# Performance work log

Hardware: AMD Instinct MI355X
Metric: run time of the kernel (lower is better)

Reference implementation:

```python
import jax, jax.numpy as jnp
import numpy as np

NUM_HEADS = 12


def setup_inputs() -> dict:
    key = jax.random.key(0)
    k1, k2, k3 = jax.random.split(key, 3)
    B, N, C = 4, 2048, 768
    x = jax.random.normal(k1, (B, N, C), dtype=jnp.float32)
    # Linear weights stored as [in, out] so y = x @ W (+ b); matches torch Linear math.
    w_qkv = jax.random.normal(k2, (C, 3 * C), dtype=jnp.float32) * (C ** -0.5)
    w_proj = jax.random.normal(k3, (C, C), dtype=jnp.float32) * (C ** -0.5)
    b_proj = jnp.zeros((C,), dtype=jnp.float32)
    return {"x": x, "w_qkv": w_qkv, "w_proj": w_proj, "b_proj": b_proj}


def reference(x, w_qkv, w_proj, b_proj):
    B, N, C = x.shape
    H = NUM_HEADS
    D = C // H
    scale = D ** -0.5
    qkv = (x @ w_qkv).reshape(B, N, 3, H, D)
    qkv = jnp.transpose(qkv, (2, 0, 3, 1, 4))  # [3, B, H, N, D]
    q, k, v = qkv[0], qkv[1], qkv[2]
    attn = jnp.einsum("bhnd,bhmd->bhnm", q, k) * scale  # [B, H, N, N]
    # causal mask (triu with offset 1), filled with -finfo.max as in the torch code
    causal_mask = jnp.triu(jnp.ones((N, N), dtype=bool), k=1)
    mask_value = -jnp.finfo(attn.dtype).max
    attn = jnp.where(causal_mask, mask_value, attn)
    attn = jax.nn.softmax(attn, axis=-1)
    attn = jnp.nan_to_num(attn)
    out = jnp.einsum("bhnm,bhmd->bhnd", attn, v)  # [B, H, N, D]
    out = jnp.transpose(out, (0, 2, 1, 3)).reshape(B, N, C)
    return out @ w_proj + b_proj
```

## Files before the change

kernel.cpp:

```cpp
#include <hip/hip_runtime.h>
#include <hip/hip_bf16.h>
#include <math.h>

#define BATCH 4
#define SEQ   2048
#define CDIM  768
#define NHEAD 12
#define HDIM  64
#define MROWS (BATCH*SEQ)
#define QKVC  (3*CDIM)

typedef __bf16    bf16x8 __attribute__((ext_vector_type(8)));
typedef _Float16  f16x8  __attribute__((ext_vector_type(8)));
typedef _Float16  f16x4  __attribute__((ext_vector_type(4)));
typedef float     f32x4  __attribute__((ext_vector_type(4)));

__device__ __forceinline__ void async16(const void* g, void* l) {
  __builtin_amdgcn_global_load_lds(
      (const __attribute__((address_space(1))) void*)g,
      (__attribute__((address_space(3))) void*)l, 16, 0, 0);
}

__global__ __launch_bounds__(256) void cast_f32_bf16(
    const float* __restrict__ in, __bf16* __restrict__ out, int n8) {
  int i = blockIdx.x * 256 + threadIdx.x;
  if (i >= n8) return;
  float4 a = reinterpret_cast<const float4*>(in)[i * 2];
  float4 b = reinterpret_cast<const float4*>(in)[i * 2 + 1];
  bf16x8 o;
  o[0] = (__bf16)a.x; o[1] = (__bf16)a.y; o[2] = (__bf16)a.z; o[3] = (__bf16)a.w;
  o[4] = (__bf16)b.x; o[5] = (__bf16)b.y; o[6] = (__bf16)b.z; o[7] = (__bf16)b.w;
  reinterpret_cast<bf16x8*>(out)[i] = o;
}

__global__ __launch_bounds__(256) void transpose_cast(
    const float* __restrict__ w, __bf16* __restrict__ wt, int K, int N) {
  __shared__ float sh[32][33];
  const int n0 = blockIdx.x * 32, k0 = blockIdx.y * 32;
  const int tx = threadIdx.x, ty = threadIdx.y;
#pragma unroll
  for (int i = 0; i < 4; ++i)
    sh[ty + i * 8][tx] = w[(size_t)(k0 + ty + i * 8) * N + n0 + tx];
  __syncthreads();
#pragma unroll
  for (int i = 0; i < 4; ++i)
    wt[(size_t)(n0 + ty + i * 8) * K + k0 + tx] = (__bf16)sh[tx][ty + i * 8];
}

template <int MODE>
__global__ __launch_bounds__(256) void gemm_bk64_kernel(
    const __bf16* __restrict__ A, const __bf16* __restrict__ Bt,
    const float* __restrict__ bias, void* __restrict__ Cout,
    __bf16* __restrict__ kF, _Float16* __restrict__ vF,
    int M, int N, int K) {
  __shared__ __align__(16) __bf16 As[2][128 * 32];
  __shared__ __align__(16) __bf16 Bs[2][128 * 32];
  const int tid  = threadIdx.x;
  const int w    = tid >> 6;
  const int lane = tid & 63;
  const int quad = lane >> 4;
  const int lr   = lane & 15;
  const int wr   = w >> 1, wc = w & 1;
  const int mBase = blockIdx.y * 128, nBase = blockIdx.x * 128;

  f32x4 acc[4][4] = {};

  const int srow = lane >> 2;
  const int sk8  = (lane & 3) * 8;
  const __bf16* aSrc0 = A  + (size_t)(mBase + w * 32 + srow) * K + sk8;
  const __bf16* aSrc1 = aSrc0 + (size_t)16 * K;
  const __bf16* bSrc0 = Bt + (size_t)(nBase + w * 32 + srow) * K + sk8;
  const __bf16* bSrc1 = bSrc0 + (size_t)16 * K;

  for (int k0 = 0; k0 < K; k0 += 64) {
    __syncthreads();
#pragma unroll
    for (int kh = 0; kh < 2; ++kh) {
      async16(aSrc0 + k0 + kh * 32, &As[kh][(w * 32 + 0) * 32]);
      async16(aSrc1 + k0 + kh * 32, &As[kh][(w * 32 + 16) * 32]);
      async16(bSrc0 + k0 + kh * 32, &Bs[kh][(w * 32 + 0) * 32]);
      async16(bSrc1 + k0 + kh * 32, &Bs[kh][(w * 32 + 16) * 32]);
    }
    __syncthreads();

#pragma unroll
    for (int kh = 0; kh < 2; ++kh) {
      bf16x8 af[4], bfr[4];
#pragma unroll
      for (int mt = 0; mt < 4; ++mt)
        af[mt] = *reinterpret_cast<const bf16x8*>(
            &As[kh][(wr * 64 + mt * 16 + lr) * 32 + quad * 8]);
#pragma unroll
      for (int nt = 0; nt < 4; ++nt)
        bfr[nt] = *reinterpret_cast<const bf16x8*>(
            &Bs[kh][(wc * 64 + nt * 16 + lr) * 32 + quad * 8]);
#pragma unroll
      for (int mt = 0; mt < 4; ++mt)
#pragma unroll
        for (int nt = 0; nt < 4; ++nt)
          acc[mt][nt] = __builtin_amdgcn_mfma_f32_16x16x32_bf16(
              af[mt], bfr[nt], acc[mt][nt], 0, 0, 0);
    }
  }

  if (MODE == 1) {
#pragma unroll
    for (int mt = 0; mt < 4; ++mt)
#pragma unroll
      for (int nt = 0; nt < 4; ++nt) {
        const int col = nBase + wc * 64 + nt * 16 + lr;
#pragma unroll
        for (int r = 0; r < 4; ++r) {
          const size_t row = (size_t)(mBase + wr * 64 + mt * 16 + quad * 4 + r);
          ((float*)Cout)[row * N + col] = acc[mt][nt][r] + bias[col];
        }
      }
  } else {
    const int region = nBase / CDIM;
    if (region == 0) {
#pragma unroll
      for (int mt = 0; mt < 4; ++mt)
#pragma unroll
        for (int nt = 0; nt < 4; ++nt) {
          const int col = nBase + wc * 64 + nt * 16 + lr;
#pragma unroll
          for (int r = 0; r < 4; ++r) {
            const size_t row = (size_t)(mBase + wr * 64 + mt * 16 + quad * 4 + r);
            ((__bf16*)Cout)[row * N + col] = (__bf16)acc[mt][nt][r];
          }
        }
    } else {
      const int bb  = mBase >> 11;
      const int ktB = ((mBase & 2047) >> 6) + wr;
      const int hq  = ((nBase % CDIM) + wc * 64) >> 6;
      const size_t tile = ((size_t)(bb * NHEAD + hq) * 32 + ktB) * 4096;
      if (region == 1) {
#pragma unroll
        for (int mt = 0; mt < 4; ++mt)
#pragma unroll
          for (int nt = 0; nt < 4; ++nt) {
            const size_t base = tile + (size_t)(mt * 2 + (nt >> 1)) * 512
                + (((nt & 1) * 2 + (lr >> 3)) * 16) * 8 + (lr & 7);
#pragma unroll
            for (int r = 0; r < 4; ++r)
              kF[base + (quad * 4 + r) * 8] = (__bf16)acc[mt][nt][r];
          }
      } else {
#pragma unroll
        for (int mt = 0; mt < 4; ++mt)
#pragma unroll
          for (int nt = 0; nt < 4; ++nt) {
            f16x4 vp;
#pragma unroll
            for (int r = 0; r < 4; ++r) vp[r] = (_Float16)acc[mt][nt][r];
            *reinterpret_cast<f16x4*>(
                &vF[tile + (size_t)(mt * 2 + (nt >> 1)) * 512
                    + (quad * 16 + lr) * 8 + (nt & 1) * 4]) = vp;
          }
      }
    }
  }
}

__global__ __launch_bounds__(256, 2) void flash_mfma_kernel(
    const __bf16* __restrict__ qkv, const __bf16* __restrict__ kF,
    const _Float16* __restrict__ vF, __bf16* __restrict__ out) {
  const int bid  = blockIdx.x;
  const int tid  = threadIdx.x;
  const int w    = tid >> 6;
  const int lane = tid & 63;
  const int quad = lane >> 4;
  const int lr   = lane & 15;

  const int x   = bid & 7;
  const int g   = bid >> 3;
  const int qt  = 31 - (g / 6);
  const int hb  = x * 6 + (g % 6);
  const int h   = hb % NHEAD, b = hb / NHEAD;

  __shared__ __align__(16) float Red[2][64 * 80];

  bf16x8 qf[4][2];
  {
    const float qs = 0.125f * 1.44269504088896f;
    const __bf16* qp = qkv + (size_t)(b * SEQ + qt * 64) * QKVC + h * HDIM;
#pragma unroll
    for (int qg = 0; qg < 4; ++qg)
#pragma unroll
      for (int kc = 0; kc < 2; ++kc) {
        bf16x8 qr = *reinterpret_cast<const bf16x8*>(
            qp + (size_t)(qg * 16 + lr) * QKVC + kc * 32 + quad * 8);
        bf16x8 f;
#pragma unroll
        for (int j = 0; j < 8; ++j) f[j] = (__bf16)((float)qr[j] * qs);
        qf[qg][kc] = f;
      }
  }

  f32x4 O[4][4] = {};
  f32x4 O4[4] = {};

  const __bf16*   kT = kF + ((size_t)(hb * 32)) * 4096 + lane * 8;
  const _Float16* vT = vF + ((size_t)(hb * 32)) * 4096 + lane * 8;
  const f16x4 vones = {(_Float16)1.f, (_Float16)1.f, (_Float16)1.f, (_Float16)1.f};

  for (int kt = w; kt <= qt; kt += 4) {
    bf16x8 kf[8];
    f16x8  vf8[8];
#pragma unroll
    for (int f = 0; f < 8; ++f)
      kf[f] = *reinterpret_cast<const bf16x8*>(kT + (size_t)kt * 4096 + f * 512);
#pragma unroll
    for (int gg = 0; gg < 8; ++gg)
      vf8[gg] = *reinterpret_cast<const f16x8*>(vT + (size_t)kt * 4096 + gg * 512);

#pragma unroll
    for (int nt = 0; nt < 4; ++nt) {
      f32x4 s[4];
#pragma unroll
      for (int qg = 0; qg < 4; ++qg) {
        f32x4 acc = (f32x4){0.f, 0.f, 0.f, 0.f};
        acc = __builtin_amdgcn_mfma_f32_16x16x32_bf16(kf[nt * 2 + 0], qf[qg][0], acc, 0, 0, 0);
        acc = __builtin_amdgcn_mfma_f32_16x16x32_bf16(kf[nt * 2 + 1], qf[qg][1], acc, 0, 0, 0);
        s[qg] = acc;
      }
      if (kt == qt) {
#pragma unroll
        for (int qg = 0; qg < 4; ++qg)
#pragma unroll
          for (int r = 0; r < 4; ++r)
            if (nt * 16 + quad * 4 + r > qg * 16 + lr) s[qg][r] = -1e30f;
      }
      f16x4 pa[4];
#pragma unroll
      for (int qg = 0; qg < 4; ++qg) {
        f16x4 t;
#pragma unroll
        for (int r = 0; r < 4; ++r)
          t[r] = (_Float16)__builtin_amdgcn_exp2f(s[qg][r]);
        pa[qg] = t;
      }
#pragma unroll
      for (int qg = 0; qg < 4; ++qg)
        O4[qg] = __builtin_amdgcn_mfma_f32_16x16x16f16(pa[qg], vones, O4[qg], 0, 0, 0);
#pragma unroll
      for (int dt = 0; dt < 4; ++dt) {
        const f16x8 vv = vf8[nt * 2 + (dt >> 1)];
        f16x4 vb;
#pragma unroll
        for (int j = 0; j < 4; ++j) vb[j] = vv[(dt & 1) * 4 + j];
#pragma unroll
        for (int qg = 0; qg < 4; ++qg)
          O[qg][dt] = __builtin_amdgcn_mfma_f32_16x16x16f16(pa[qg], vb, O[qg][dt], 0, 0, 0);
      }
    }
  }

  if (w == 1 || w == 3) {
    float* dst = Red[w >> 1];
#pragma unroll
    for (int qg = 0; qg < 4; ++qg)
#pragma unroll
      for (int dt = 0; dt < 4; ++dt)
        *reinterpret_cast<f32x4*>(&dst[((qg * 4 + dt) * 64 + lane) * 4]) = O[qg][dt];
#pragma unroll
    for (int qg = 0; qg < 4; ++qg)
      *reinterpret_cast<f32x4*>(&dst[((16 + qg) * 64 + lane) * 4]) = O4[qg];
  }
  __syncthreads();
  if (w == 0 || w == 2) {
    const float* src = Red[w >> 1];
#pragma unroll
    for (int qg = 0; qg < 4; ++qg)
#pragma unroll
      for (int dt = 0; dt < 4; ++dt)
        O[qg][dt] += *reinterpret_cast<const f32x4*>(&src[((qg * 4 + dt) * 64 + lane) * 4]);
#pragma unroll
    for (int qg = 0; qg < 4; ++qg)
      O4[qg] += *reinterpret_cast<const f32x4*>(&src[((16 + qg) * 64 + lane) * 4]);
  }
  __syncthreads();
  if (w == 2) {
    float* dst = Red[0];
#pragma unroll
    for (int qg = 0; qg < 4; ++qg)
#pragma unroll
      for (int dt = 0; dt < 4; ++dt)
        *reinterpret_cast<f32x4*>(&dst[((qg * 4 + dt) * 64 + lane) * 4]) = O[qg][dt];
#pragma unroll
    for (int qg = 0; qg < 4; ++qg)
      *reinterpret_cast<f32x4*>(&dst[((16 + qg) * 64 + lane) * 4]) = O4[qg];
  }
  __syncthreads();
  if (w == 0) {
    const float* src = Red[0];
#pragma unroll
    for (int qg = 0; qg < 4; ++qg)
#pragma unroll
      for (int dt = 0; dt < 4; ++dt)
        O[qg][dt] += *reinterpret_cast<const f32x4*>(&src[((qg * 4 + dt) * 64 + lane) * 4]);
#pragma unroll
    for (int qg = 0; qg < 4; ++qg)
      O4[qg] += *reinterpret_cast<const f32x4*>(&src[((16 + qg) * 64 + lane) * 4]);

    __bf16* obase = out + (size_t)(b * SEQ + qt * 64) * CDIM + h * HDIM;
#pragma unroll
    for (int qg = 0; qg < 4; ++qg) {
      float linv[4];
#pragma unroll
      for (int r = 0; r < 4; ++r) linv[r] = 1.f / O4[qg][r];
#pragma unroll
      for (int dt = 0; dt < 4; ++dt)
#pragma unroll
        for (int r = 0; r < 4; ++r)
          obase[(size_t)(qg * 16 + quad * 4 + r) * CDIM + dt * 16 + lr] =
              (__bf16)(O[qg][dt][r] * linv[r]);
    }
  }
}

extern "C" void kernel_launch(void* const* d_in, const int* in_sizes, int n_in,
                              void* d_out, int out_size, void* d_ws, size_t ws_size,
                              hipStream_t stream) {
  const float* x      = (const float*)d_in[0];
  const float* w_qkv  = (const float*)d_in[1];
  const float* w_proj = (const float*)d_in[2];
  const float* b_proj = (const float*)d_in[3];
  float* out = (float*)d_out;

  __bf16* qkv    = (__bf16*)d_ws;
  __bf16* attnb  = qkv + (size_t)MROWS * QKVC;
  __bf16* xb     = attnb + (size_t)MROWS * CDIM;
  __bf16* wqkvT  = xb + (size_t)MROWS * CDIM;
  __bf16* wprojT = wqkvT + (size_t)QKVC * CDIM;
  __bf16* kFb    = wprojT + (size_t)CDIM * CDIM;
  _Float16* vFb  = (_Float16*)(kFb + (size_t)48 * 32 * 4096);

  cast_f32_bf16<<<dim3((MROWS * CDIM / 8 + 255) / 256), dim3(256), 0, stream>>>(
      x, xb, MROWS * CDIM / 8);
  transpose_cast<<<dim3(QKVC / 32, CDIM / 32), dim3(32, 8), 0, stream>>>(
      w_qkv, wqkvT, CDIM, QKVC);
  transpose_cast<<<dim3(CDIM / 32, CDIM / 32), dim3(32, 8), 0, stream>>>(
      w_proj, wprojT, CDIM, CDIM);

  gemm_bk64_kernel<0><<<dim3(QKVC / 128, MROWS / 128), dim3(256), 0, stream>>>(
      xb, wqkvT, nullptr, qkv, kFb, vFb, MROWS, QKVC, CDIM);

  flash_mfma_kernel<<<dim3(1536), dim3(256), 0, stream>>>(qkv, kFb, vFb, attnb);

  gemm_bk64_kernel<1><<<dim3(CDIM / 128, MROWS / 128), dim3(256), 0, stream>>>(
      attnb, wprojT, b_proj, out, nullptr, nullptr, MROWS, CDIM, CDIM);
}
```

Baseline: 195.3 us.

## Pair causal query tiles per block, merge prep kernels, pack exp conversion

The flash attention kernel now processes two query tiles per block (tile 31-p and tile p), so every block does a balanced amount of causal work and the grid is halved to 768 blocks. The three preprocessing launches (x cast and two weight transposes) are merged into one prep kernel to cut launch overhead. The exp-to-half conversion uses packed round-toward-zero cvt_pkrtz instead of per-element casts. The trade-off is fewer blocks for the scheduler to spread across CUs, a slight rounding change in the probabilities, and an extra barrier per phase.

```diff
diff --git a/kernel.cpp b/kernel.cpp
--- a/kernel.cpp
+++ b/kernel.cpp
@@ -14,6 +14,7 @@
 typedef _Float16  f16x8  __attribute__((ext_vector_type(8)));
 typedef _Float16  f16x4  __attribute__((ext_vector_type(4)));
 typedef float     f32x4  __attribute__((ext_vector_type(4)));
+typedef __fp16    hf16x2 __attribute__((ext_vector_type(2)));
 
 __device__ __forceinline__ void async16(const void* g, void* l) {
   __builtin_amdgcn_global_load_lds(
@@ -21,30 +22,44 @@
       (__attribute__((address_space(3))) void*)l, 16, 0, 0);
 }
 
-__global__ __launch_bounds__(256) void cast_f32_bf16(
-    const float* __restrict__ in, __bf16* __restrict__ out, int n8) {
-  int i = blockIdx.x * 256 + threadIdx.x;
-  if (i >= n8) return;
-  float4 a = reinterpret_cast<const float4*>(in)[i * 2];
-  float4 b = reinterpret_cast<const float4*>(in)[i * 2 + 1];
-  bf16x8 o;
-  o[0] = (__bf16)a.x; o[1] = (__bf16)a.y; o[2] = (__bf16)a.z; o[3] = (__bf16)a.w;
-  o[4] = (__bf16)b.x; o[5] = (__bf16)b.y; o[6] = (__bf16)b.z; o[7] = (__bf16)b.w;
-  reinterpret_cast<bf16x8*>(out)[i] = o;
-}
-
-__global__ __launch_bounds__(256) void transpose_cast(
-    const float* __restrict__ w, __bf16* __restrict__ wt, int K, int N) {
+__global__ __launch_bounds__(256) void prep_kernel(
+    const float* __restrict__ x, __bf16* __restrict__ xb,
+    const float* __restrict__ w_qkv, __bf16* __restrict__ wqkvT,
+    const float* __restrict__ w_proj, __bf16* __restrict__ wprojT) {
   __shared__ float sh[32][33];
-  const int n0 = blockIdx.x * 32, k0 = blockIdx.y * 32;
-  const int tx = threadIdx.x, ty = threadIdx.y;
+  const int bid = blockIdx.x;
+  const int tid = threadIdx.x;
+
+  if (bid < 3072) {
+    const int i = bid * 256 + tid;
+    float4 a = reinterpret_cast<const float4*>(x)[i * 2];
+    float4 b = reinterpret_cast<const float4*>(x)[i * 2 + 1];
+    bf16x8 o;
+    o[0] = (__bf16)a.x; o[1] = (__bf16)a.y; o[2] = (__bf16)a.z; o[3] = (__bf16)a.w;
+    o[4] = (__bf16)b.x; o[5] = (__bf16)b.y; o[6] = (__bf16)b.z; o[7] = (__bf16)b.w;
+    reinterpret_cast<bf16x8*>(xb)[i] = o;
+    return;
+  }
+  const float* w;
+  __bf16* wt;
+  int n0, k0, N;
+  if (bid < 4800) {
+    const int t = bid - 3072;
+    w = w_qkv; wt = wqkvT; N = QKVC;
+    n0 = (t % 72) * 32; k0 = (t / 72) * 32;
+  } else {
+    const int t = bid - 4800;
+    w = w_proj; wt = wprojT; N = CDIM;
+    n0 = (t % 24) * 32; k0 = (t / 24) * 32;
+  }
+  const int tx = tid & 31, ty = tid >> 5;
 #pragma unroll
   for (int i = 0; i < 4; ++i)
     sh[ty + i * 8][tx] = w[(size_t)(k0 + ty + i * 8) * N + n0 + tx];
   __syncthreads();
 #pragma unroll
   for (int i = 0; i < 4; ++i)
-    wt[(size_t)(n0 + ty + i * 8) * K + k0 + tx] = (__bf16)sh[tx][ty + i * 8];
+    wt[(size_t)(n0 + ty + i * 8) * CDIM + k0 + tx] = (__bf16)sh[tx][ty + i * 8];
 }
 
 template <int MODE>
@@ -174,147 +189,153 @@
 
   const int x   = bid & 7;
   const int g   = bid >> 3;
-  const int qt  = 31 - (g / 6);
+  const int p   = g / 6;
   const int hb  = x * 6 + (g % 6);
   const int h   = hb % NHEAD, b = hb / NHEAD;
 
   __shared__ __align__(16) float Red[2][64 * 80];
-
-  bf16x8 qf[4][2];
-  {
-    const float qs = 0.125f * 1.44269504088896f;
-    const __bf16* qp = qkv + (size_t)(b * SEQ + qt * 64) * QKVC + h * HDIM;
-#pragma unroll
-    for (int qg = 0; qg < 4; ++qg)
-#pragma unroll
-      for (int kc = 0; kc < 2; ++kc) {
-        bf16x8 qr = *reinterpret_cast<const bf16x8*>(
-            qp + (size_t)(qg * 16 + lr) * QKVC + kc * 32 + quad * 8);
-        bf16x8 f;
-#pragma unroll
-        for (int j = 0; j < 8; ++j) f[j] = (__bf16)((float)qr[j] * qs);
-        qf[qg][kc] = f;
-      }
-  }
-
-  f32x4 O[4][4] = {};
-  f32x4 O4[4] = {};
 
   const __bf16*   kT = kF + ((size_t)(hb * 32)) * 4096 + lane * 8;
   const _Float16* vT = vF + ((size_t)(hb * 32)) * 4096 + lane * 8;
   const f16x4 vones = {(_Float16)1.f, (_Float16)1.f, (_Float16)1.f, (_Float16)1.f};
 
-  for (int kt = w; kt <= qt; kt += 4) {
-    bf16x8 kf[8];
-    f16x8  vf8[8];
-#pragma unroll
-    for (int f = 0; f < 8; ++f)
-      kf[f] = *reinterpret_cast<const bf16x8*>(kT + (size_t)kt * 4096 + f * 512);
-#pragma unroll
-    for (int gg = 0; gg < 8; ++gg)
-      vf8[gg] = *reinterpret_cast<const f16x8*>(vT + (size_t)kt * 4096 + gg * 512);
-
-#pragma unroll
-    for (int nt = 0; nt < 4; ++nt) {
-      f32x4 s[4];
+  for (int phase = 0; phase < 2; ++phase) {
+    const int qt = phase ? p : 31 - p;
+
+    bf16x8 qf[4][2];
+    {
+      const float qs = 0.125f * 1.44269504088896f;
+      const __bf16* qp = qkv + (size_t)(b * SEQ + qt * 64) * QKVC + h * HDIM;
+#pragma unroll
+      for (int qg = 0; qg < 4; ++qg)
+#pragma unroll
+        for (int kc = 0; kc < 2; ++kc) {
+          bf16x8 qr = *reinterpret_cast<const bf16x8*>(
+              qp + (size_t)(qg * 16 + lr) * QKVC + kc * 32 + quad * 8);
+          bf16x8 f;
+#pragma unroll
+          for (int j = 0; j < 8; ++j) f[j] = (__bf16)((float)qr[j] * qs);
+          qf[qg][kc] = f;
+        }
+    }
+
+    f32x4 O[4][4] = {};
+    f32x4 O4[4] = {};
+
+    for (int kt = w; kt <= qt; kt += 4) {
+      bf16x8 kf[8];
+      f16x8  vf8[8];
+#pragma unroll
+      for (int f = 0; f < 8; ++f)
+        kf[f] = *reinterpret_cast<const bf16x8*>(kT + (size_t)kt * 4096 + f * 512);
+#pragma unroll
+      for (int gg = 0; gg < 8; ++gg)
+        vf8[gg] = *reinterpret_cast<const f16x8*>(vT + (size_t)kt * 4096 + gg * 512);
+
+#pragma unroll
+      for (int nt = 0; nt < 4; ++nt) {
+        f32x4 s[4];
+#pragma unroll
+        for (int qg = 0; qg < 4; ++qg) {
+          f32x4 acc = (f32x4){0.f, 0.f, 0.f, 0.f};
+          acc = __builtin_amdgcn_mfma_f32_16x16x32_bf16(kf[nt * 2 + 0], qf[qg][0], acc, 0, 0, 0);
+          acc = __builtin_amdgcn_mfma_f32_16x16x32_bf16(kf[nt * 2 + 1], qf[qg][1], acc, 0, 0, 0);
+          s[qg] = acc;
+        }
+        if (kt == qt) {
+#pragma unroll
+          for (int qg = 0; qg < 4; ++qg)
+#pragma unroll
+            for (int r = 0; r < 4; ++r)
+              if (nt * 16 + quad * 4 + r > qg * 16 + lr) s[qg][r] = -1e30f;
+        }
+        f16x4 pa[4];
+#pragma unroll
+        for (int qg = 0; qg < 4; ++qg) {
+          union { hf16x2 h[2]; f16x4 v; } u;
+          u.h[0] = __builtin_amdgcn_cvt_pkrtz(
+              __builtin_amdgcn_exp2f(s[qg][0]), __builtin_amdgcn_exp2f(s[qg][1]));
+          u.h[1] = __builtin_amdgcn_cvt_pkrtz(
+              __builtin_amdgcn_exp2f(s[qg][2]), __builtin_amdgcn_exp2f(s[qg][3]));
+          pa[qg] = u.v;
+        }
+#pragma unroll
+        for (int qg = 0; qg < 4; ++qg)
+          O4[qg] = __builtin_amdgcn_mfma_f32_16x16x16f16(pa[qg], vones, O4[qg], 0, 0, 0);
+#pragma unroll
+        for (int dt = 0; dt < 4; ++dt) {
+          const f16x8 vv = vf8[nt * 2 + (dt >> 1)];
+          f16x4 vb;
+#pragma unroll
+          for (int j = 0; j < 4; ++j) vb[j] = vv[(dt & 1) * 4 + j];
+#pragma unroll
+          for (int qg = 0; qg < 4; ++qg)
+            O[qg][dt] = __builtin_amdgcn_mfma_f32_16x16x16f16(pa[qg], vb, O[qg][dt], 0, 0, 0);
+        }
+      }
+    }
+
+    __syncthreads();
+    if (w == 1 || w == 3) {
+      float* dst = Red[w >> 1];
+#pragma unroll
+      for (int qg = 0; qg < 4; ++qg)
+#pragma unroll
+        for (int dt = 0; dt < 4; ++dt)
+          *reinterpret_cast<f32x4*>(&dst[((qg * 4 + dt) * 64 + lane) * 4]) = O[qg][dt];
+#pragma unroll
+      for (int qg = 0; qg < 4; ++qg)
+        *reinterpret_cast<f32x4*>(&dst[((16 + qg) * 64 + lane) * 4]) = O4[qg];
+    }
+    __syncthreads();
+    if (w == 0 || w == 2) {
+      const float* src = Red[w >> 1];
+#pragma unroll
+      for (int qg = 0; qg < 4; ++qg)
+#pragma unroll
+        for (int dt = 0; dt < 4; ++dt)
+          O[qg][dt] += *reinterpret_cast<const f32x4*>(&src[((qg * 4 + dt) * 64 + lane) * 4]);
+#pragma unroll
+      for (int qg = 0; qg < 4; ++qg)
+        O4[qg] += *reinterpret_cast<const f32x4*>(&src[((16 + qg) * 64 + lane) * 4]);
+    }
+    __syncthreads();
+    if (w == 2) {
+      float* dst = Red[0];
+#pragma unroll
+      for (int qg = 0; qg < 4; ++qg)
+#pragma unroll
+        for (int dt = 0; dt < 4; ++dt)
+          *reinterpret_cast<f32x4*>(&dst[((qg * 4 + dt) * 64 + lane) * 4]) = O[qg][dt];
+#pragma unroll
+      for (int qg = 0; qg < 4; ++qg)
+        *reinterpret_cast<f32x4*>(&dst[((16 + qg) * 64 + lane) * 4]) = O4[qg];
+    }
+    __syncthreads();
+    if (w == 0) {
+      const float* src = Red[0];
+#pragma unroll
+      for (int qg = 0; qg < 4; ++qg)
+#pragma unroll
+        for (int dt = 0; dt < 4; ++dt)
+          O[qg][dt] += *reinterpret_cast<const f32x4*>(&src[((qg * 4 + dt) * 64 + lane) * 4]);
+#pragma unroll
+      for (int qg = 0; qg < 4; ++qg)
+        O4[qg] += *reinterpret_cast<const f32x4*>(&src[((16 + qg) * 64 + lane) * 4]);
+
+      __bf16* obase = out + (size_t)(b * SEQ + qt * 64) * CDIM + h * HDIM;
 #pragma unroll
       for (int qg = 0; qg < 4; ++qg) {
-        f32x4 acc = (f32x4){0.f, 0.f, 0.f, 0.f};
-        acc = __builtin_amdgcn_mfma_f32_16x16x32_bf16(kf[nt * 2 + 0], qf[qg][0], acc, 0, 0, 0);
-        acc = __builtin_amdgcn_mfma_f32_16x16x32_bf16(kf[nt * 2 + 1], qf[qg][1], acc, 0, 0, 0);
-        s[qg] = acc;
+        float linv[4];
+#pragma unroll
+        for (int r = 0; r < 4; ++r) linv[r] = 1.f / O4[qg][r];
+#pragma unroll
+        for (int dt = 0; dt < 4; ++dt)
+#pragma unroll
+          for (int r = 0; r < 4; ++r)
+            obase[(size_t)(qg * 16 + quad * 4 + r) * CDIM + dt * 16 + lr] =
+                (__bf16)(O[qg][dt][r] * linv[r]);
       }
-      if (kt == qt) {
-#pragma unroll
-        for (int qg = 0; qg < 4; ++qg)
-#pragma unroll
-          for (int r = 0; r < 4; ++r)
-            if (nt * 16 + quad * 4 + r > qg * 16 + lr) s[qg][r] = -1e30f;
-      }
-      f16x4 pa[4];
-#pragma unroll
-      for (int qg = 0; qg < 4; ++qg) {
-        f16x4 t;
-#pragma unroll
-        for (int r = 0; r < 4; ++r)
-          t[r] = (_Float16)__builtin_amdgcn_exp2f(s[qg][r]);
-        pa[qg] = t;
-      }
-#pragma unroll
-      for (int qg = 0; qg < 4; ++qg)
-        O4[qg] = __builtin_amdgcn_mfma_f32_16x16x16f16(pa[qg], vones, O4[qg], 0, 0, 0);
-#pragma unroll
-      for (int dt = 0; dt < 4; ++dt) {
-        const f16x8 vv = vf8[nt * 2 + (dt >> 1)];
-        f16x4 vb;
-#pragma unroll
-        for (int j = 0; j < 4; ++j) vb[j] = vv[(dt & 1) * 4 + j];
-#pragma unroll
-        for (int qg = 0; qg < 4; ++qg)
-          O[qg][dt] = __builtin_amdgcn_mfma_f32_16x16x16f16(pa[qg], vb, O[qg][dt], 0, 0, 0);
-      }
-    }
-  }
-
-  if (w == 1 || w == 3) {
-    float* dst = Red[w >> 1];
-#pragma unroll
-    for (int qg = 0; qg < 4; ++qg)
-#pragma unroll
-      for (int dt = 0; dt < 4; ++dt)
-        *reinterpret_cast<f32x4*>(&dst[((qg * 4 + dt) * 64 + lane) * 4]) = O[qg][dt];
-#pragma unroll
-    for (int qg = 0; qg < 4; ++qg)
-      *reinterpret_cast<f32x4*>(&dst[((16 + qg) * 64 + lane) * 4]) = O4[qg];
-  }
-  __syncthreads();
-  if (w == 0 || w == 2) {
-    const float* src = Red[w >> 1];
-#pragma unroll
-    for (int qg = 0; qg < 4; ++qg)
-#pragma unroll
-      for (int dt = 0; dt < 4; ++dt)
-        O[qg][dt] += *reinterpret_cast<const f32x4*>(&src[((qg * 4 + dt) * 64 + lane) * 4]);
-#pragma unroll
-    for (int qg = 0; qg < 4; ++qg)
-      O4[qg] += *reinterpret_cast<const f32x4*>(&src[((16 + qg) * 64 + lane) * 4]);
-  }
-  __syncthreads();
-  if (w == 2) {
-    float* dst = Red[0];
-#pragma unroll
-    for (int qg = 0; qg < 4; ++qg)
-#pragma unroll
-      for (int dt = 0; dt < 4; ++dt)
-        *reinterpret_cast<f32x4*>(&dst[((qg * 4 + dt) * 64 + lane) * 4]) = O[qg][dt];
-#pragma unroll
-    for (int qg = 0; qg < 4; ++qg)
-      *reinterpret_cast<f32x4*>(&dst[((16 + qg) * 64 + lane) * 4]) = O4[qg];
-  }
-  __syncthreads();
-  if (w == 0) {
-    const float* src = Red[0];
-#pragma unroll
-    for (int qg = 0; qg < 4; ++qg)
-#pragma unroll
-      for (int dt = 0; dt < 4; ++dt)
-        O[qg][dt] += *reinterpret_cast<const f32x4*>(&src[((qg * 4 + dt) * 64 + lane) * 4]);
-#pragma unroll
-    for (int qg = 0; qg < 4; ++qg)
-      O4[qg] += *reinterpret_cast<const f32x4*>(&src[((16 + qg) * 64 + lane) * 4]);
-
-    __bf16* obase = out + (size_t)(b * SEQ + qt * 64) * CDIM + h * HDIM;
-#pragma unroll
-    for (int qg = 0; qg < 4; ++qg) {
-      float linv[4];
-#pragma unroll
-      for (int r = 0; r < 4; ++r) linv[r] = 1.f / O4[qg][r];
-#pragma unroll
-      for (int dt = 0; dt < 4; ++dt)
-#pragma unroll
-        for (int r = 0; r < 4; ++r)
-          obase[(size_t)(qg * 16 + quad * 4 + r) * CDIM + dt * 16 + lr] =
-              (__bf16)(O[qg][dt][r] * linv[r]);
     }
   }
 }
@@ -336,17 +357,13 @@
   __bf16* kFb    = wprojT + (size_t)CDIM * CDIM;
   _Float16* vFb  = (_Float16*)(kFb + (size_t)48 * 32 * 4096);
 
-  cast_f32_bf16<<<dim3((MROWS * CDIM / 8 + 255) / 256), dim3(256), 0, stream>>>(
-      x, xb, MROWS * CDIM / 8);
-  transpose_cast<<<dim3(QKVC / 32, CDIM / 32), dim3(32, 8), 0, stream>>>(
-      w_qkv, wqkvT, CDIM, QKVC);
-  transpose_cast<<<dim3(CDIM / 32, CDIM / 32), dim3(32, 8), 0, stream>>>(
-      w_proj, wprojT, CDIM, CDIM);
+  prep_kernel<<<dim3(5376), dim3(256), 0, stream>>>(
+      x, xb, w_qkv, wqkvT, w_proj, wprojT);
 
   gemm_bk64_kernel<0><<<dim3(QKVC / 128, MROWS / 128), dim3(256), 0, stream>>>(
       xb, wqkvT, nullptr, qkv, kFb, vFb, MROWS, QKVC, CDIM);
 
-  flash_mfma_kernel<<<dim3(1536), dim3(256), 0, stream>>>(qkv, kFb, vFb, attnb);
+  flash_mfma_kernel<<<dim3(768), dim3(256), 0, stream>>>(qkv, kFb, vFb, attnb);
 
   gemm_bk64_kernel<1><<<dim3(CDIM / 128, MROWS / 128), dim3(256), 0, stream>>>(
       attnb, wprojT, b_proj, out, nullptr, nullptr, MROWS, CDIM, CDIM);
```

Result: no change. 198.6 us (+1.7%).
